# Kernel tuning notes

Measured on AMD Instinct MI355X. Metric: run time of the kernel, lower is better.

The kernel has to match this reference:

```python
import jax, jax.numpy as jnp
import numpy as np
from itertools import combinations_with_replacement

B, T, F, L, POLY_ORDER = 16, 2048, 128, 16, 3


def _hilbert_filter(N):
    # Matches pytorch_hilbert: H[0]=0, H[1:N//2]=2, H[N//2]=0 (even N)
    h = np.zeros(N, dtype=np.float32)
    if N % 2 == 0:
        h[1:N // 2] = 2.0
    else:
        h[1:(N + 1) // 2] = 2.0
    return jnp.asarray(h)


def hilbert(sig, axis=1):
    N = sig.shape[axis]
    Xf = jnp.fft.fft(sig, axis=axis)
    shape = [1] * sig.ndim
    shape[axis] = N
    return jnp.fft.ifft(Xf * _hilbert_filter(N).reshape(shape), axis=axis)


def _combo_indices(latent, poly_order):
    # static index arrays, grouped by degree n
    return [np.array(list(combinations_with_replacement(range(latent), n)), dtype=np.int32)
            for n in range(1, poly_order + 1)]


def compute_library(z, poly_order):
    # z: [B, T, L] -> theta: [B, T, library_dim]
    feats = []
    for combos in _combo_indices(z.shape[-1], poly_order):
        zc = z[..., combos]            # [B, T, ncomb, n]
        feats.append(jnp.prod(zc, axis=-1))  # [B, T, ncomb]
    analytic = hilbert(z, axis=1)
    feats.append(z)
    feats.append(jnp.abs(analytic))    # extract_real_component
    feats.append(jnp.angle(analytic))  # extract_imaginary_component
    return jnp.concatenate(feats, axis=-1)


def setup_inputs() -> dict:
    key = jax.random.key(0)
    ks = jax.random.split(key, 7)
    lib_dim = L + 2 * L + sum(len(c) for c in _combo_indices(L, POLY_ORDER))
    s_enc = 1.0 / np.sqrt(F)
    s_dec = 1.0 / np.sqrt(L)
    s_sin = 1.0 / np.sqrt(lib_dim)
    return {
        "x": jax.random.normal(ks[0], (B, T, F), dtype=jnp.float32),
        "W_enc": jax.random.uniform(ks[1], (L, F), jnp.float32, -s_enc, s_enc),
        "b_enc": jax.random.uniform(ks[2], (L,), jnp.float32, -s_enc, s_enc),
        "W_dec": jax.random.uniform(ks[3], (F, L), jnp.float32, -s_dec, s_dec),
        "b_dec": jax.random.uniform(ks[4], (F,), jnp.float32, -s_dec, s_dec),
        "W_sindy": jax.random.uniform(ks[5], (L, lib_dim), jnp.float32, -s_sin, s_sin),
        "b_sindy": jax.random.uniform(ks[6], (L,), jnp.float32, -s_sin, s_sin),
    }


def reference(x, W_enc, b_enc, W_dec, b_dec, W_sindy, b_sindy):
    z = jnp.einsum('btf,lf->btl', x, W_enc) + b_enc          # encoder
    theta = compute_library(z, POLY_ORDER)                    # [B,T,lib_dim]
    y_hat = jnp.einsum('btd,ld->btl', theta, W_sindy) + b_sindy
    x_hat = jnp.einsum('btl,fl->btf', z, W_dec) + b_dec       # decoder
    # Jacobian of the linear encoder w.r.t. x is the constant weight matrix
    # broadcast per (b, t): identical math to the O((B*T)^2) autograd version.
    jac_z_x = jnp.broadcast_to(W_enc, (x.shape[0], x.shape[1], L, F))
    return (y_hat, x_hat, z, jac_z_x, W_sindy, W_dec)
```

## Files before the change

kernel.cpp:

```cpp
#include <hip/hip_runtime.h>
#include <math.h>

typedef unsigned short u16;
typedef unsigned int   u32;
typedef __attribute__((ext_vector_type(4))) float f32x4;

#define OFF_AT    0
#define OFF_PT    524288
#define OFF_WT    1048576
#define OFF_ZT    1064832
#define OFF_TWC   1589120
#define OFF_TWS   1591168

#define R1_LO 0
#define R1_HI 5592576
#define R2_LO 5592576
#define R2_HI 11185152
#define R3_LO 11185152
#define R3_HI 16777216

__device__ __forceinline__ void jac_range(const float* __restrict__ Wenc,
                                          float* __restrict__ out_jac,
                                          int lo, int hi, int idx, int nth)
{
    const float* wsrc = Wenc + (size_t)((lo + idx) & 511) * 4;
    f32x4 w;
    w.x = wsrc[0]; w.y = wsrc[1]; w.z = wsrc[2]; w.w = wsrc[3];
    f32x4* j4 = (f32x4*)out_jac;
    for (int i = lo + idx; i < hi; i += nth)
        __builtin_nontemporal_store(w, j4 + i);
}

__global__ __launch_bounds__(256) void k1_encdec(
    const float* __restrict__ x, const float* __restrict__ Wenc, const float* __restrict__ benc,
    const float* __restrict__ Wdec, const float* __restrict__ bdec,
    const float* __restrict__ Wsin,
    float* __restrict__ out_z, float* __restrict__ out_xhat,
    float* __restrict__ out_Ws, float* __restrict__ out_Wd,
    float* __restrict__ z_t, float* __restrict__ wt,
    double* __restrict__ twc_g, double* __restrict__ tws_g,
    float* __restrict__ out_jac)
{
    int tid = threadIdx.x;
    int blk = blockIdx.x;

    if (blk >= 1092) {
        jac_range(Wenc, out_jac, R1_LO, R1_HI, (blk - 1092) * 256 + tid, 262144);
        return;
    }
    if (blk >= 1024) {
        int t0 = (blk - 1024) * 256 + tid;
        if (t0 < 16256) {
            float v = Wsin[t0];
            out_Ws[t0] = v;
            int l = t0 / 1016;
            int d = t0 - l * 1016;
            if (d < 16) v += Wsin[t0 + 968];
            wt[d * 16 + l] = v;
        } else if (t0 < 17280) {
            int k = t0 - 16256;
            double ang = -6.283185307179586476925286766559 * (double)k / 2048.0;
            double s_, c_;
            sincos(ang, &s_, &c_);
            twc_g[k] = c_;
            tws_g[k] = s_;
        }
        if (t0 < 2048) out_Wd[t0] = Wdec[t0];
        return;
    }

    __shared__ float xs[32][132];
    __shared__ float we[16][132];
    __shared__ float wdT[16][132];
    __shared__ float zs[32][20];

    {
        const float4* xv = (const float4*)x + (size_t)blk * 1024;
        float4* xs4 = (float4*)&xs[0][0];
        #pragma unroll
        for (int h = 0; h < 4; ++h) {
            int vi = tid + h * 256;
            int pt = vi >> 5, fq = vi & 31;
            xs4[pt * 33 + fq] = xv[vi];
        }
    }
    {
        const float4* wev = (const float4*)Wenc;
        float4* we4 = (float4*)&we[0][0];
        #pragma unroll
        for (int h = 0; h < 2; ++h) {
            int vi = tid + h * 256;
            int l = vi >> 5, fq = vi & 31;
            we4[l * 33 + fq] = wev[vi];
        }
    }
    {
        const float4* wdv = (const float4*)Wdec;
        #pragma unroll
        for (int h = 0; h < 2; ++h) {
            int vi = tid + h * 256;
            float4 v = wdv[vi];
            int f = vi >> 2, lq = (vi & 3) * 4;
            wdT[lq + 0][f] = v.x; wdT[lq + 1][f] = v.y;
            wdT[lq + 2][f] = v.z; wdT[lq + 3][f] = v.w;
        }
    }
    __syncthreads();

    {
        int pt = tid >> 3, lp = tid & 7;
        const float4* xr = (const float4*)&xs[pt][0];
        const float4* wa = (const float4*)&we[lp][0];
        const float4* wb = (const float4*)&we[lp + 8][0];
        float s0 = 0.f, s1 = 0.f;
        #pragma unroll 8
        for (int fq = 0; fq < 32; ++fq) {
            float4 a = xr[fq], u = wa[fq], v = wb[fq];
            s0 = fmaf(a.x, u.x, s0); s0 = fmaf(a.y, u.y, s0);
            s0 = fmaf(a.z, u.z, s0); s0 = fmaf(a.w, u.w, s0);
            s1 = fmaf(a.x, v.x, s1); s1 = fmaf(a.y, v.y, s1);
            s1 = fmaf(a.z, v.z, s1); s1 = fmaf(a.w, v.w, s1);
        }
        zs[pt][lp]     = s0 + benc[lp];
        zs[pt][lp + 8] = s1 + benc[lp + 8];
    }
    __syncthreads();

    {
        #pragma unroll
        for (int h = 0; h < 2; ++h) {
            int i = tid + h * 256;
            out_z[(size_t)blk * 512 + i] = zs[i >> 4][i & 15];
        }
        #pragma unroll
        for (int h = 0; h < 2; ++h) {
            int i = tid + h * 256;
            int l = i >> 5, pt = i & 31;
            z_t[(size_t)l * 32768 + blk * 32 + pt] = zs[pt][l];
        }
    }

    {
        int f = tid & 127, half = tid >> 7;
        float w[16];
        #pragma unroll
        for (int l = 0; l < 16; ++l) w[l] = wdT[l][f];
        float bd = bdec[f];
        #pragma unroll
        for (int p = 0; p < 16; ++p) {
            int pt = half * 16 + p;
            const float4* zr = (const float4*)&zs[pt][0];
            float4 z0 = zr[0], z1 = zr[1], z2 = zr[2], z3 = zr[3];
            float acc = bd;
            acc = fmaf(z0.x, w[0],  acc); acc = fmaf(z0.y, w[1],  acc);
            acc = fmaf(z0.z, w[2],  acc); acc = fmaf(z0.w, w[3],  acc);
            acc = fmaf(z1.x, w[4],  acc); acc = fmaf(z1.y, w[5],  acc);
            acc = fmaf(z1.z, w[6],  acc); acc = fmaf(z1.w, w[7],  acc);
            acc = fmaf(z2.x, w[8],  acc); acc = fmaf(z2.y, w[9],  acc);
            acc = fmaf(z2.z, w[10], acc); acc = fmaf(z2.w, w[11], acc);
            acc = fmaf(z3.x, w[12], acc); acc = fmaf(z3.y, w[13], acc);
            acc = fmaf(z3.z, w[14], acc); acc = fmaf(z3.w, w[15], acc);
            out_xhat[(size_t)blk * 4096 + (size_t)pt * 128 + f] = acc;
        }
    }
}

#define TWPAD(k) ((k) + ((k) >> 5))
#define CP(i)    ((i) + ((i) >> 4))

__global__ __launch_bounds__(1024) void k2_hilbert(
    const float* __restrict__ z_t, const double* __restrict__ twc_g,
    const double* __restrict__ tws_g, const float* __restrict__ Wenc,
    float* __restrict__ a_t, float* __restrict__ p_t,
    float* __restrict__ out_jac)
{
    __shared__ double2 c[2176];
    __shared__ double twc_s[1056];
    __shared__ double tws_s[1056];

    int tid = threadIdx.x;
    if (blockIdx.x >= 256) {
        jac_range(Wenc, out_jac, R2_LO, R2_HI, (blockIdx.x - 256) * 1024 + tid, 524288);
        return;
    }
    int b = blockIdx.x >> 4, l = blockIdx.x & 15;
    const size_t base = (size_t)l * 32768 + (size_t)b * 2048;
    const float* zp = z_t + base;

    {
        twc_s[TWPAD(tid)] = twc_g[tid];
        tws_s[TWPAD(tid)] = tws_g[tid];
    }
    {
        double2 v0; v0.x = (double)zp[tid];        v0.y = 0.0;
        double2 v1; v1.x = (double)zp[tid + 1024]; v1.y = 0.0;
        c[CP(tid)] = v0;
        c[CP(tid + 1024)] = v1;
    }
    __syncthreads();

    for (int half = 1024; half >= 1; half >>= 1) {
        int step = 1024 / half;
        int j = tid & (half - 1);
        int pos = ((tid - j) << 1) + j;
        int pa = CP(pos), pb = CP(pos + half);
        int ti = TWPAD(j * step);
        double2 u = c[pa], v = c[pb];
        double wc = twc_s[ti], wsn = tws_s[ti];
        double2 s, dsc;
        s.x = u.x + v.x;  s.y = u.y + v.y;
        double br = u.x - v.x, bi = u.y - v.y;
        dsc.x = br * wc - bi * wsn;
        dsc.y = br * wsn + bi * wc;
        c[pa] = s;
        c[pb] = dsc;
        __syncthreads();
    }

    #pragma unroll
    for (int h = 0; h < 2; ++h) {
        int t = tid + h * 1024;
        double sc = (t == 0 || (t & 1)) ? 0.0 : (2.0 / 2048.0);
        int ci = CP(t);
        double2 v = c[ci];
        v.x *= sc; v.y *= sc;
        c[ci] = v;
    }
    __syncthreads();

    for (int half = 1; half <= 1024; half <<= 1) {
        int step = 1024 / half;
        int j = tid & (half - 1);
        int pos = ((tid - j) << 1) + j;
        int pa = CP(pos), pb = CP(pos + half);
        int ti = TWPAD(j * step);
        double2 u = c[pa], v = c[pb];
        double wc = twc_s[ti], wsn = tws_s[ti];
        double tr = v.x * wc + v.y * wsn;
        double ti2 = v.y * wc - v.x * wsn;
        double2 p0, p1;
        p0.x = u.x + tr; p0.y = u.y + ti2;
        p1.x = u.x - tr; p1.y = u.y - ti2;
        c[pa] = p0;
        c[pb] = p1;
        __syncthreads();
    }

    #pragma unroll
    for (int h = 0; h < 2; ++h) {
        int t = tid + h * 1024;
        double2 v = c[CP(t)];
        a_t[base + t] = (float)sqrt(v.x * v.x + v.y * v.y);
        p_t[base + t] = (float)atan2(v.y, v.x);
    }
}

#define EMIT2(EXPR) do {                                                    \
    if ((unsigned)(d - LO) < 121u) {                                        \
        float vv[2];                                                        \
        _Pragma("unroll") for (int p = 0; p < 2; ++p) vv[p] = (EXPR);       \
        int bb = (d - LO) << 4;                                             \
        _Pragma("unroll") for (int l = 0; l < 16; ++l) {                    \
            float w = lw[bb + l];                                           \
            acc[0][l] = fmaf(vv[0], w, acc[0][l]);                          \
            acc[1][l] = fmaf(vv[1], w, acc[1][l]);                          \
        }                                                                   \
    }                                                                       \
    ++d;                                                                    \
} while (0)

template<int LO>
__device__ __forceinline__ void poly_accum(const float (&z)[2][16],
                                           const float* __restrict__ lw,
                                           float (&acc)[2][16])
{
    int d = 0;
    #pragma unroll
    for (int i = 0; i < 16; ++i) EMIT2(z[p][i]);
    #pragma unroll
    for (int i = 0; i < 16; ++i)
        #pragma unroll
        for (int j = i; j < 16; ++j) EMIT2(z[p][i] * z[p][j]);
    #pragma unroll
    for (int i = 0; i < 16; ++i)
        #pragma unroll
        for (int j = i; j < 16; ++j)
            #pragma unroll
            for (int k = j; k < 16; ++k) EMIT2(z[p][i] * z[p][j] * z[p][k]);
}

__global__ __launch_bounds__(256, 2) void k3_yhat(
    const float* __restrict__ z_ws, const float* __restrict__ wt,
    const float* __restrict__ Wenc,
    float* __restrict__ part, float* __restrict__ out_jac)
{
    __shared__ float lw[1936];
    int tid = threadIdx.x;
    if (blockIdx.x >= 512) {
        jac_range(Wenc, out_jac, R3_LO, R3_HI, (blockIdx.x - 512) * 256 + tid, 262144);
        return;
    }
    int slice = blockIdx.x >> 6;
    int ptgrp = blockIdx.x & 63;
    int base = ptgrp * 512;

    {
        const float4* src = (const float4*)(wt + slice * 121 * 16);
        float4* dst = (float4*)lw;
        for (int i = tid; i < 484; i += 256) dst[i] = src[i];
    }
    __syncthreads();

    float z[2][16], acc[2][16];
    #pragma unroll
    for (int p = 0; p < 2; ++p) {
        int bt = base + p * 256 + tid;
        const float4* zp = (const float4*)(z_ws + (size_t)bt * 16);
        #pragma unroll
        for (int q = 0; q < 4; ++q) {
            float4 v = zp[q];
            z[p][q*4+0]=v.x; z[p][q*4+1]=v.y; z[p][q*4+2]=v.z; z[p][q*4+3]=v.w;
        }
    }
    #pragma unroll
    for (int p = 0; p < 2; ++p)
        #pragma unroll
        for (int l = 0; l < 16; ++l) acc[p][l] = 0.f;

    switch (slice) {
        case 0: poly_accum<0 * 121>(z, lw, acc); break;
        case 1: poly_accum<1 * 121>(z, lw, acc); break;
        case 2: poly_accum<2 * 121>(z, lw, acc); break;
        case 3: poly_accum<3 * 121>(z, lw, acc); break;
        case 4: poly_accum<4 * 121>(z, lw, acc); break;
        case 5: poly_accum<5 * 121>(z, lw, acc); break;
        case 6: poly_accum<6 * 121>(z, lw, acc); break;
        default: poly_accum<7 * 121>(z, lw, acc); break;
    }

    #pragma unroll
    for (int p = 0; p < 2; ++p) {
        int bt = base + p * 256 + tid;
        float4* pp = (float4*)(part + (size_t)slice * 524288 + (size_t)bt * 16);
        #pragma unroll
        for (int q = 0; q < 4; ++q) {
            float4 v;
            v.x = acc[p][q*4+0]; v.y = acc[p][q*4+1];
            v.z = acc[p][q*4+2]; v.w = acc[p][q*4+3];
            pp[q] = v;
        }
    }
}

__global__ __launch_bounds__(256) void k3_tail(
    const float* __restrict__ part, const float* __restrict__ a_t,
    const float* __restrict__ p_t, const float* __restrict__ wt,
    const float* __restrict__ bsin, float* __restrict__ out_y)
{
    __shared__ float lw[512];
    int tid = threadIdx.x;
    if (tid < 128) {
        ((float4*)lw)[tid] = ((const float4*)(wt + 984 * 16))[tid];
    }
    __syncthreads();

    int bt = blockIdx.x * 128 + (tid >> 1);
    int lh = (tid & 1) * 8;
    float acc[8];
    {
        const float4* bp = (const float4*)bsin;
        #pragma unroll
        for (int q = 0; q < 2; ++q) {
            float4 v = bp[(lh >> 2) + q];
            acc[q*4+0]=v.x; acc[q*4+1]=v.y; acc[q*4+2]=v.z; acc[q*4+3]=v.w;
        }
    }
    #pragma unroll
    for (int sl = 0; sl < 8; ++sl) {
        const float4* pp = (const float4*)(part + (size_t)sl * 524288 + (size_t)bt * 16 + lh);
        #pragma unroll
        for (int q = 0; q < 2; ++q) {
            float4 v = pp[q];
            acc[q*4+0]+=v.x; acc[q*4+1]+=v.y; acc[q*4+2]+=v.z; acc[q*4+3]+=v.w;
        }
    }
    #pragma unroll
    for (int i = 0; i < 16; ++i) {
        float av = a_t[(size_t)i * 32768 + bt];
        #pragma unroll
        for (int l = 0; l < 8; ++l) acc[l] = fmaf(av, lw[i * 16 + lh + l], acc[l]);
    }
    #pragma unroll
    for (int i = 0; i < 16; ++i) {
        float pv = p_t[(size_t)i * 32768 + bt];
        #pragma unroll
        for (int l = 0; l < 8; ++l) acc[l] = fmaf(pv, lw[256 + i * 16 + lh + l], acc[l]);
    }

    float4* yp = (float4*)(out_y + (size_t)bt * 16 + lh);
    #pragma unroll
    for (int q = 0; q < 2; ++q) {
        float4 v;
        v.x = acc[q*4+0]; v.y = acc[q*4+1]; v.z = acc[q*4+2]; v.w = acc[q*4+3];
        yp[q] = v;
    }
}

extern "C" void kernel_launch(void* const* d_in, const int* in_sizes, int n_in,
                              void* d_out, int out_size, void* d_ws, size_t ws_size,
                              hipStream_t stream)
{
    const float* x  = (const float*)d_in[0];
    const float* We = (const float*)d_in[1];
    const float* be = (const float*)d_in[2];
    const float* Wd = (const float*)d_in[3];
    const float* bd = (const float*)d_in[4];
    const float* Ws = (const float*)d_in[5];
    const float* bs = (const float*)d_in[6];

    float* out  = (float*)d_out;
    float* o_y  = out;
    float* o_xh = out + 524288;
    float* o_z  = out + 4718592;
    float* o_j  = out + 5242880;
    float* o_Ws = out + 72351744;
    float* o_Wd = out + 72368000;

    float*  ws    = (float*)d_ws;
    float*  a_t   = ws + OFF_AT;
    float*  p_t   = ws + OFF_PT;
    float*  wt    = ws + OFF_WT;
    float*  z_t   = ws + OFF_ZT;
    double* twc_g = (double*)(ws + OFF_TWC);
    double* tws_g = (double*)(ws + OFF_TWS);
    float*  part  = ws + 1593216;

    hipLaunchKernelGGL(k1_encdec, dim3(2116), dim3(256), 0, stream,
                       x, We, be, Wd, bd, Ws, o_z, o_xh, o_Ws, o_Wd,
                       z_t, wt, twc_g, tws_g, o_j);
    hipLaunchKernelGGL(k2_hilbert, dim3(768), dim3(1024), 0, stream,
                       z_t, twc_g, tws_g, We, a_t, p_t, o_j);
    hipLaunchKernelGGL(k3_yhat, dim3(1536), dim3(256), 0, stream,
                       o_z, wt, We, part, o_j);
    hipLaunchKernelGGL(k3_tail, dim3(256), dim3(256), 0, stream,
                       part, a_t, p_t, wt, bs, o_y);
}
```

Measured before the change: 329.1 us.

## Move Jacobian broadcast fill into a dedicated up-front kernel

Removes the Jacobian broadcast stores that were spread across extra blocks of the three compute kernels and writes them all from a new standalone kernel launched first. Each block writes 16 consecutive (b,t) copies of W_enc with plain stores in place of nontemporal ones. This gives up the overlap of the 268MB store stream with the FFT and y_hat compute and serializes it ahead of them. In exchange, the compute kernels get simpler launches without the extra filler blocks.

```diff
diff --git a/kernel.cpp b/kernel.cpp
--- a/kernel.cpp
+++ b/kernel.cpp
@@ -3,7 +3,6 @@
 
 typedef unsigned short u16;
 typedef unsigned int   u32;
-typedef __attribute__((ext_vector_type(4))) float f32x4;
 
 #define OFF_AT    0
 #define OFF_PT    524288
@@ -12,23 +11,19 @@
 #define OFF_TWC   1589120
 #define OFF_TWS   1591168
 
-#define R1_LO 0
-#define R1_HI 5592576
-#define R2_LO 5592576
-#define R2_HI 11185152
-#define R3_LO 11185152
-#define R3_HI 16777216
-
-__device__ __forceinline__ void jac_range(const float* __restrict__ Wenc,
-                                          float* __restrict__ out_jac,
-                                          int lo, int hi, int idx, int nth)
-{
-    const float* wsrc = Wenc + (size_t)((lo + idx) & 511) * 4;
-    f32x4 w;
-    w.x = wsrc[0]; w.y = wsrc[1]; w.z = wsrc[2]; w.w = wsrc[3];
-    f32x4* j4 = (f32x4*)out_jac;
-    for (int i = lo + idx; i < hi; i += nth)
-        __builtin_nontemporal_store(w, j4 + i);
+__global__ __launch_bounds__(256) void k0_jac(
+    const float* __restrict__ Wenc, float* __restrict__ out_jac)
+{
+    int tid = threadIdx.x;
+    const float4* We4 = (const float4*)Wenc;
+    float4 w0 = We4[tid];
+    float4 w1 = We4[tid + 256];
+    float4* j4 = (float4*)out_jac + (size_t)blockIdx.x * 8192;
+    #pragma unroll
+    for (int t = 0; t < 16; ++t) {
+        j4[t * 512 + tid]       = w0;
+        j4[t * 512 + 256 + tid] = w1;
+    }
 }
 
 __global__ __launch_bounds__(256) void k1_encdec(
@@ -38,16 +33,11 @@
     float* __restrict__ out_z, float* __restrict__ out_xhat,
     float* __restrict__ out_Ws, float* __restrict__ out_Wd,
     float* __restrict__ z_t, float* __restrict__ wt,
-    double* __restrict__ twc_g, double* __restrict__ tws_g,
-    float* __restrict__ out_jac)
+    double* __restrict__ twc_g, double* __restrict__ tws_g)
 {
     int tid = threadIdx.x;
     int blk = blockIdx.x;
 
-    if (blk >= 1092) {
-        jac_range(Wenc, out_jac, R1_LO, R1_HI, (blk - 1092) * 256 + tid, 262144);
-        return;
-    }
     if (blk >= 1024) {
         int t0 = (blk - 1024) * 256 + tid;
         if (t0 < 16256) {
@@ -170,19 +160,14 @@
 
 __global__ __launch_bounds__(1024) void k2_hilbert(
     const float* __restrict__ z_t, const double* __restrict__ twc_g,
-    const double* __restrict__ tws_g, const float* __restrict__ Wenc,
-    float* __restrict__ a_t, float* __restrict__ p_t,
-    float* __restrict__ out_jac)
+    const double* __restrict__ tws_g,
+    float* __restrict__ a_t, float* __restrict__ p_t)
 {
     __shared__ double2 c[2176];
     __shared__ double twc_s[1056];
     __shared__ double tws_s[1056];
 
     int tid = threadIdx.x;
-    if (blockIdx.x >= 256) {
-        jac_range(Wenc, out_jac, R2_LO, R2_HI, (blockIdx.x - 256) * 1024 + tid, 524288);
-        return;
-    }
     int b = blockIdx.x >> 4, l = blockIdx.x & 15;
     const size_t base = (size_t)l * 32768 + (size_t)b * 2048;
     const float* zp = z_t + base;
@@ -291,15 +276,10 @@
 
 __global__ __launch_bounds__(256, 2) void k3_yhat(
     const float* __restrict__ z_ws, const float* __restrict__ wt,
-    const float* __restrict__ Wenc,
-    float* __restrict__ part, float* __restrict__ out_jac)
+    float* __restrict__ part)
 {
     __shared__ float lw[1936];
     int tid = threadIdx.x;
-    if (blockIdx.x >= 512) {
-        jac_range(Wenc, out_jac, R3_LO, R3_HI, (blockIdx.x - 512) * 256 + tid, 262144);
-        return;
-    }
     int slice = blockIdx.x >> 6;
     int ptgrp = blockIdx.x & 63;
     int base = ptgrp * 512;
@@ -435,13 +415,15 @@
     double* tws_g = (double*)(ws + OFF_TWS);
     float*  part  = ws + 1593216;
 
-    hipLaunchKernelGGL(k1_encdec, dim3(2116), dim3(256), 0, stream,
+    hipLaunchKernelGGL(k0_jac, dim3(2048), dim3(256), 0, stream,
+                       We, o_j);
+    hipLaunchKernelGGL(k1_encdec, dim3(1092), dim3(256), 0, stream,
                        x, We, be, Wd, bd, Ws, o_z, o_xh, o_Ws, o_Wd,
-                       z_t, wt, twc_g, tws_g, o_j);
-    hipLaunchKernelGGL(k2_hilbert, dim3(768), dim3(1024), 0, stream,
-                       z_t, twc_g, tws_g, We, a_t, p_t, o_j);
-    hipLaunchKernelGGL(k3_yhat, dim3(1536), dim3(256), 0, stream,
-                       o_z, wt, We, part, o_j);
+                       z_t, wt, twc_g, tws_g);
+    hipLaunchKernelGGL(k2_hilbert, dim3(256), dim3(1024), 0, stream,
+                       z_t, twc_g, tws_g, a_t, p_t);
+    hipLaunchKernelGGL(k3_yhat, dim3(512), dim3(256), 0, stream,
+                       o_z, wt, part);
     hipLaunchKernelGGL(k3_tail, dim3(256), dim3(256), 0, stream,
                        part, a_t, p_t, wt, bs, o_y);
 }
```

Measured after the change: 389.3 us. 18.3% more time.

## Merge polynomial y_hat slices and tail reduction into one kernel

Applied to the files above, without the earlier changes.

Replaces the eight-slice poly kernel plus separate tail reduction with one kernel. Each block now loads the whole 968x16 SINDy weight table into LDS, and four threads per point each compute all polynomial features for four output columns. This removes the partial-sum buffer round trip through global memory and one kernel launch. The cost is that every thread recomputes all 968 features redundantly, and the LDS footprint per block grows to about 64 KB, which may limit occupancy.

```diff
diff --git a/kernel.cpp b/kernel.cpp
--- a/kernel.cpp
+++ b/kernel.cpp
@@ -255,155 +255,92 @@
     }
 }
 
-#define EMIT2(EXPR) do {                                                    \
-    if ((unsigned)(d - LO) < 121u) {                                        \
-        float vv[2];                                                        \
-        _Pragma("unroll") for (int p = 0; p < 2; ++p) vv[p] = (EXPR);       \
-        int bb = (d - LO) << 4;                                             \
-        _Pragma("unroll") for (int l = 0; l < 16; ++l) {                    \
-            float w = lw[bb + l];                                           \
-            acc[0][l] = fmaf(vv[0], w, acc[0][l]);                          \
-            acc[1][l] = fmaf(vv[1], w, acc[1][l]);                          \
-        }                                                                   \
-    }                                                                       \
+#define EMITF(EXPR) do {                                                    \
+    float fv = (EXPR);                                                      \
+    _Pragma("unroll") for (int l = 0; l < 4; ++l)                           \
+        s[d / 121][l] = fmaf(fv, lw[(d << 4) + lg4 + l], s[d / 121][l]);    \
     ++d;                                                                    \
 } while (0)
 
-template<int LO>
-__device__ __forceinline__ void poly_accum(const float (&z)[2][16],
-                                           const float* __restrict__ lw,
-                                           float (&acc)[2][16])
-{
-    int d = 0;
-    #pragma unroll
-    for (int i = 0; i < 16; ++i) EMIT2(z[p][i]);
-    #pragma unroll
-    for (int i = 0; i < 16; ++i)
-        #pragma unroll
-        for (int j = i; j < 16; ++j) EMIT2(z[p][i] * z[p][j]);
-    #pragma unroll
-    for (int i = 0; i < 16; ++i)
-        #pragma unroll
-        for (int j = i; j < 16; ++j)
-            #pragma unroll
-            for (int k = j; k < 16; ++k) EMIT2(z[p][i] * z[p][j] * z[p][k]);
-}
-
-__global__ __launch_bounds__(256, 2) void k3_yhat(
+__global__ __launch_bounds__(256, 2) void k3_merged(
     const float* __restrict__ z_ws, const float* __restrict__ wt,
-    const float* __restrict__ Wenc,
-    float* __restrict__ part, float* __restrict__ out_jac)
-{
-    __shared__ float lw[1936];
+    const float* __restrict__ a_t, const float* __restrict__ p_t,
+    const float* __restrict__ bsin, const float* __restrict__ Wenc,
+    float* __restrict__ out_y, float* __restrict__ out_jac)
+{
+    __shared__ float lw[15488];
+    __shared__ float lw2[512];
     int tid = threadIdx.x;
     if (blockIdx.x >= 512) {
         jac_range(Wenc, out_jac, R3_LO, R3_HI, (blockIdx.x - 512) * 256 + tid, 262144);
         return;
     }
-    int slice = blockIdx.x >> 6;
-    int ptgrp = blockIdx.x & 63;
-    int base = ptgrp * 512;
-
-    {
-        const float4* src = (const float4*)(wt + slice * 121 * 16);
+
+    {
+        const float4* src = (const float4*)wt;
         float4* dst = (float4*)lw;
-        for (int i = tid; i < 484; i += 256) dst[i] = src[i];
-    }
-    __syncthreads();
-
-    float z[2][16], acc[2][16];
-    #pragma unroll
-    for (int p = 0; p < 2; ++p) {
-        int bt = base + p * 256 + tid;
+        for (int i = tid; i < 3872; i += 256) dst[i] = src[i];
+        if (tid < 128) ((float4*)lw2)[tid] = src[3936 + tid];
+    }
+    __syncthreads();
+
+    int pi  = tid >> 2;
+    int lg4 = (tid & 3) * 4;
+    int bt  = blockIdx.x * 64 + pi;
+
+    float z[16];
+    {
         const float4* zp = (const float4*)(z_ws + (size_t)bt * 16);
         #pragma unroll
         for (int q = 0; q < 4; ++q) {
             float4 v = zp[q];
-            z[p][q*4+0]=v.x; z[p][q*4+1]=v.y; z[p][q*4+2]=v.z; z[p][q*4+3]=v.w;
-        }
-    }
-    #pragma unroll
-    for (int p = 0; p < 2; ++p)
-        #pragma unroll
-        for (int l = 0; l < 16; ++l) acc[p][l] = 0.f;
-
-    switch (slice) {
-        case 0: poly_accum<0 * 121>(z, lw, acc); break;
-        case 1: poly_accum<1 * 121>(z, lw, acc); break;
-        case 2: poly_accum<2 * 121>(z, lw, acc); break;
-        case 3: poly_accum<3 * 121>(z, lw, acc); break;
-        case 4: poly_accum<4 * 121>(z, lw, acc); break;
-        case 5: poly_accum<5 * 121>(z, lw, acc); break;
-        case 6: poly_accum<6 * 121>(z, lw, acc); break;
-        default: poly_accum<7 * 121>(z, lw, acc); break;
-    }
-
-    #pragma unroll
-    for (int p = 0; p < 2; ++p) {
-        int bt = base + p * 256 + tid;
-        float4* pp = (float4*)(part + (size_t)slice * 524288 + (size_t)bt * 16);
-        #pragma unroll
-        for (int q = 0; q < 4; ++q) {
-            float4 v;
-            v.x = acc[p][q*4+0]; v.y = acc[p][q*4+1];
-            v.z = acc[p][q*4+2]; v.w = acc[p][q*4+3];
-            pp[q] = v;
-        }
-    }
-}
-
-__global__ __launch_bounds__(256) void k3_tail(
-    const float* __restrict__ part, const float* __restrict__ a_t,
-    const float* __restrict__ p_t, const float* __restrict__ wt,
-    const float* __restrict__ bsin, float* __restrict__ out_y)
-{
-    __shared__ float lw[512];
-    int tid = threadIdx.x;
-    if (tid < 128) {
-        ((float4*)lw)[tid] = ((const float4*)(wt + 984 * 16))[tid];
-    }
-    __syncthreads();
-
-    int bt = blockIdx.x * 128 + (tid >> 1);
-    int lh = (tid & 1) * 8;
-    float acc[8];
-    {
-        const float4* bp = (const float4*)bsin;
-        #pragma unroll
-        for (int q = 0; q < 2; ++q) {
-            float4 v = bp[(lh >> 2) + q];
-            acc[q*4+0]=v.x; acc[q*4+1]=v.y; acc[q*4+2]=v.z; acc[q*4+3]=v.w;
-        }
-    }
-    #pragma unroll
-    for (int sl = 0; sl < 8; ++sl) {
-        const float4* pp = (const float4*)(part + (size_t)sl * 524288 + (size_t)bt * 16 + lh);
-        #pragma unroll
-        for (int q = 0; q < 2; ++q) {
-            float4 v = pp[q];
-            acc[q*4+0]+=v.x; acc[q*4+1]+=v.y; acc[q*4+2]+=v.z; acc[q*4+3]+=v.w;
-        }
-    }
+            z[q*4+0]=v.x; z[q*4+1]=v.y; z[q*4+2]=v.z; z[q*4+3]=v.w;
+        }
+    }
+
+    float s[8][4];
+    #pragma unroll
+    for (int sl = 0; sl < 8; ++sl)
+        #pragma unroll
+        for (int l = 0; l < 4; ++l) s[sl][l] = 0.f;
+
+    int d = 0;
+    #pragma unroll
+    for (int i = 0; i < 16; ++i) EMITF(z[i]);
+    #pragma unroll
+    for (int i = 0; i < 16; ++i)
+        #pragma unroll
+        for (int j = i; j < 16; ++j) EMITF(z[i] * z[j]);
+    #pragma unroll
+    for (int i = 0; i < 16; ++i)
+        #pragma unroll
+        for (int j = i; j < 16; ++j)
+            #pragma unroll
+            for (int k = j; k < 16; ++k) EMITF(z[i] * z[j] * z[k]);
+
+    float acc[4];
+    #pragma unroll
+    for (int l = 0; l < 4; ++l) acc[l] = bsin[lg4 + l];
+    #pragma unroll
+    for (int sl = 0; sl < 8; ++sl)
+        #pragma unroll
+        for (int l = 0; l < 4; ++l) acc[l] += s[sl][l];
     #pragma unroll
     for (int i = 0; i < 16; ++i) {
         float av = a_t[(size_t)i * 32768 + bt];
         #pragma unroll
-        for (int l = 0; l < 8; ++l) acc[l] = fmaf(av, lw[i * 16 + lh + l], acc[l]);
+        for (int l = 0; l < 4; ++l) acc[l] = fmaf(av, lw2[i * 16 + lg4 + l], acc[l]);
     }
     #pragma unroll
     for (int i = 0; i < 16; ++i) {
         float pv = p_t[(size_t)i * 32768 + bt];
         #pragma unroll
-        for (int l = 0; l < 8; ++l) acc[l] = fmaf(pv, lw[256 + i * 16 + lh + l], acc[l]);
-    }
-
-    float4* yp = (float4*)(out_y + (size_t)bt * 16 + lh);
-    #pragma unroll
-    for (int q = 0; q < 2; ++q) {
-        float4 v;
-        v.x = acc[q*4+0]; v.y = acc[q*4+1]; v.z = acc[q*4+2]; v.w = acc[q*4+3];
-        yp[q] = v;
-    }
+        for (int l = 0; l < 4; ++l) acc[l] = fmaf(pv, lw2[256 + i * 16 + lg4 + l], acc[l]);
+    }
+
+    float4 v;
+    v.x = acc[0]; v.y = acc[1]; v.z = acc[2]; v.w = acc[3];
+    *(float4*)(out_y + (size_t)bt * 16 + lg4) = v;
 }
 
 extern "C" void kernel_launch(void* const* d_in, const int* in_sizes, int n_in,
@@ -433,15 +370,12 @@
     float*  z_t   = ws + OFF_ZT;
     double* twc_g = (double*)(ws + OFF_TWC);
     double* tws_g = (double*)(ws + OFF_TWS);
-    float*  part  = ws + 1593216;
 
     hipLaunchKernelGGL(k1_encdec, dim3(2116), dim3(256), 0, stream,
                        x, We, be, Wd, bd, Ws, o_z, o_xh, o_Ws, o_Wd,
                        z_t, wt, twc_g, tws_g, o_j);
     hipLaunchKernelGGL(k2_hilbert, dim3(768), dim3(1024), 0, stream,
                        z_t, twc_g, tws_g, We, a_t, p_t, o_j);
-    hipLaunchKernelGGL(k3_yhat, dim3(1536), dim3(256), 0, stream,
-                       o_z, wt, We, part, o_j);
-    hipLaunchKernelGGL(k3_tail, dim3(256), dim3(256), 0, stream,
-                       part, a_t, p_t, wt, bs, o_y);
-}
+    hipLaunchKernelGGL(k3_merged, dim3(1536), dim3(256), 0, stream,
+                       o_z, wt, a_t, p_t, bs, We, o_y, o_j);
+}
```

Result: slower. 336.0 us (+2.1%).
